# Performance work log

Hardware: AMD Instinct MI355X
Metric: run time of the kernel (lower is better)

Reference implementation:

```python
import jax, jax.numpy as jnp
import numpy as np
from jax import lax

T_LEN, BATCH, D_IN, D_HID, N_LAYERS = 512, 32, 512, 512, 4


def setup_inputs() -> dict:
    key = jax.random.key(0)
    kx, kw, ku = jax.random.split(key, 3)
    x = jax.random.normal(kx, (T_LEN, BATCH, D_IN), dtype=jnp.float32)
    # xavier-ish scale on input kernels to keep the relu recurrence stable
    W = jax.random.normal(kw, (N_LAYERS, D_HID, D_IN), dtype=jnp.float32) * (1.0 / np.sqrt(D_IN))
    b = jnp.zeros((N_LAYERS, D_HID), dtype=jnp.float32)
    # diagonal recurrent weights in [0,1) so |u|<=1 (non-exploding)
    u = jax.random.uniform(ku, (N_LAYERS, D_HID), dtype=jnp.float32)
    return {"x": x, "W": W, "b": b, "u": u}


def _indrnn_layer(x, W_l, b_l, u_l):
    # x: [T, B, Din]; precompute input projection as one big GEMM
    xh = jnp.einsum('tbd,hd->tbh', x, W_l) + b_l  # [T, B, Dh]
    h0 = jnp.zeros((x.shape[1], W_l.shape[0]), dtype=x.dtype)

    def step(h, xh_t):
        h_new = jax.nn.relu(xh_t + u_l * h)
        return h_new, h_new

    _, outs = lax.scan(step, h0, xh)
    return outs  # [T, B, Dh]


def reference(x, W, b, u):
    out = x
    for l in range(W.shape[0]):  # fixed small layer count
        out = _indrnn_layer(out, W[l], b[l], u[l])
    return out
```

## Files before the change

kernel.cpp:

```cpp
#include <hip/hip_runtime.h>
#include <hip/hip_bf16.h>

typedef short bf16x8 __attribute__((ext_vector_type(8)));
typedef float f32x4 __attribute__((ext_vector_type(4)));

#define T_LEN 512
#define BATCH 32
#define D 512
#define M_TOT (T_LEN * BATCH)
#define NLAYER 4

#define BM 128
#define BN 128
#define BK 64
#define NT (D / BK)
#define EP 72

#define CH 32
#define NCH (T_LEN / CH)

__global__ __launch_bounds__(256) void convert_k(const float* __restrict__ W,
                                                 __hip_bfloat16* __restrict__ Wb) {
    const int i = (blockIdx.x * 256 + threadIdx.x) * 4;
    float4 v = *(const float4*)(W + i);
    __hip_bfloat16 h0 = __float2bfloat16(v.x);
    __hip_bfloat16 h1 = __float2bfloat16(v.y);
    __hip_bfloat16 h2 = __float2bfloat16(v.z);
    __hip_bfloat16 h3 = __float2bfloat16(v.w);
    ushort4 o;
    o.x = *(const unsigned short*)&h0;
    o.y = *(const unsigned short*)&h1;
    o.z = *(const unsigned short*)&h2;
    o.w = *(const unsigned short*)&h3;
    *(ushort4*)(Wb + i) = o;
}

template <bool AF32>
__global__ __launch_bounds__(256) void gemm_bt(const void* __restrict__ Avp,
                                               const __hip_bfloat16* __restrict__ Bt,
                                               const float* __restrict__ bias,
                                               __hip_bfloat16* __restrict__ Cb) {
    constexpr int K = D;
    constexpr int N = D;
    __shared__ __hip_bfloat16 smem[4 * BM * BK];
    __hip_bfloat16* const AsP[2] = {smem, smem + BM * BK};
    __hip_bfloat16* const BsP[2] = {smem + 2 * BM * BK, smem + 3 * BM * BK};

    const int tid  = threadIdx.x;
    const int wave = tid >> 6;
    const int lane = tid & 63;

    const int bid = blockIdx.x;
    const int xcd = bid & 7;
    const int jb  = bid >> 3;
    const int bm  = xcd * 16 + (jb >> 2);
    const int bn  = jb & 3;

    const int wm = (wave >> 1) * 64;
    const int wn = (wave & 1) * 64;

    const int srow = lane >> 3;
    const int scol = ((lane & 7) ^ srow) * 8;

    const __hip_bfloat16* Ag = AF32 ? nullptr
                                    : (const __hip_bfloat16*)Avp + (size_t)(bm * BM) * K;
    const float* Agf = AF32 ? (const float*)Avp + (size_t)(bm * BM) * K : nullptr;
    const __hip_bfloat16* Bg = Bt + (size_t)(bn * BN) * K;

    f32x4 acc[4][4] = {};
    float4 va[4][2];

#define STAGE_A_LDS(buf, k0)                                                                         \
    do {                                                                                             \
        _Pragma("unroll") for (int jj = 0; jj < 4; ++jj) {                                           \
            const int rbase = (jj * 4 + wave) * 8;                                                   \
            __builtin_amdgcn_global_load_lds(                                                        \
                (const __attribute__((address_space(1))) void*)(Ag + (size_t)(rbase + srow) * K + (k0) + scol), \
                (__attribute__((address_space(3))) void*)(&AsP[buf][rbase * BK]), 16, 0, 0);         \
        }                                                                                            \
    } while (0)

#define STAGE_B(buf, k0)                                                                             \
    do {                                                                                             \
        _Pragma("unroll") for (int jj = 0; jj < 4; ++jj) {                                           \
            const int rbase = (jj * 4 + wave) * 8;                                                   \
            __builtin_amdgcn_global_load_lds(                                                        \
                (const __attribute__((address_space(1))) void*)(Bg + (size_t)(rbase + srow) * K + (k0) + scol), \
                (__attribute__((address_space(3))) void*)(&BsP[buf][rbase * BK]), 16, 0, 0);         \
        }                                                                                            \
    } while (0)

#define LOAD_A_F32(k0)                                                                               \
    do {                                                                                             \
        _Pragma("unroll") for (int jj = 0; jj < 4; ++jj) {                                           \
            const int rbase = (jj * 4 + wave) * 8;                                                   \
            const float* s = Agf + (size_t)(rbase + srow) * K + (k0) + scol;                         \
            va[jj][0] = *(const float4*)s;                                                           \
            va[jj][1] = *(const float4*)(s + 4);                                                     \
        }                                                                                            \
    } while (0)

#define WRITE_A_F32(buf)                                                                             \
    do {                                                                                             \
        _Pragma("unroll") for (int jj = 0; jj < 4; ++jj) {                                           \
            const int rbase = (jj * 4 + wave) * 8;                                                   \
            bf16x8 pk;                                                                               \
            _Pragma("unroll") for (int q = 0; q < 4; ++q) {                                          \
                __hip_bfloat16 t0 = __float2bfloat16(((const float*)&va[jj][0])[q]);                 \
                __hip_bfloat16 t1 = __float2bfloat16(((const float*)&va[jj][1])[q]);                 \
                pk[q]     = *(const short*)&t0;                                                      \
                pk[q + 4] = *(const short*)&t1;                                                      \
            }                                                                                        \
            *(bf16x8*)(&AsP[buf][(rbase + srow) * BK + (lane & 7) * 8]) = pk;                        \
        }                                                                                            \
    } while (0)

#define COMPUTE(buf)                                                                                 \
    do {                                                                                             \
        bf16x8 af[4][2], bv[4][2];                                                                   \
        const int fr = lane & 15;                                                                    \
        const int kq = lane >> 4;                                                                    \
        _Pragma("unroll") for (int mi = 0; mi < 4; ++mi) {                                           \
            const int r = wm + mi * 16 + fr;                                                         \
            _Pragma("unroll") for (int kh = 0; kh < 2; ++kh) {                                       \
                const int c = ((kh * 4 + kq) ^ (fr & 7)) * 8;                                        \
                af[mi][kh] = *(const bf16x8*)(&AsP[buf][r * BK + c]);                                \
            }                                                                                        \
        }                                                                                            \
        _Pragma("unroll") for (int ni = 0; ni < 4; ++ni) {                                           \
            const int r = wn + ni * 16 + fr;                                                         \
            _Pragma("unroll") for (int kh = 0; kh < 2; ++kh) {                                       \
                const int c = ((kh * 4 + kq) ^ (fr & 7)) * 8;                                        \
                bv[ni][kh] = *(const bf16x8*)(&BsP[buf][r * BK + c]);                                \
            }                                                                                        \
        }                                                                                            \
        _Pragma("unroll") for (int kh = 0; kh < 2; ++kh)                                             \
            _Pragma("unroll") for (int mi = 0; mi < 4; ++mi)                                         \
                _Pragma("unroll") for (int ni = 0; ni < 4; ++ni)                                     \
                    acc[mi][ni] = __builtin_amdgcn_mfma_f32_16x16x32_bf16(af[mi][kh], bv[ni][kh],    \
                                                                          acc[mi][ni], 0, 0, 0);    \
    } while (0)

    if constexpr (AF32) {
        LOAD_A_F32(0);
        STAGE_B(0, 0);
        WRITE_A_F32(0);
        __syncthreads();
        int cur = 0;
#pragma unroll
        for (int kt = 1; kt < NT; ++kt) {
            LOAD_A_F32(kt * BK);
            STAGE_B(cur ^ 1, kt * BK);
            COMPUTE(cur);
            WRITE_A_F32(cur ^ 1);
            __syncthreads();
            cur ^= 1;
        }
        COMPUTE(cur);
    } else {
        STAGE_A_LDS(0, 0);
        STAGE_B(0, 0);
        __syncthreads();
        int cur = 0;
#pragma unroll
        for (int kt = 1; kt < NT; ++kt) {
            STAGE_A_LDS(cur ^ 1, kt * BK);
            STAGE_B(cur ^ 1, kt * BK);
            COMPUTE(cur);
            __syncthreads();
            cur ^= 1;
        }
        COMPUTE(cur);
    }
    __syncthreads();

    {
        __hip_bfloat16* S = smem + wave * (64 * EP);
        const int cfr = lane & 15;
        const int cfq = lane >> 4;
        float bs[4];
#pragma unroll
        for (int ni = 0; ni < 4; ++ni) bs[ni] = bias[bn * BN + wn + ni * 16 + cfr];
#pragma unroll
        for (int mi = 0; mi < 4; ++mi)
#pragma unroll
            for (int ni = 0; ni < 4; ++ni)
#pragma unroll
                for (int r = 0; r < 4; ++r)
                    S[(mi * 16 + cfq * 4 + r) * EP + ni * 16 + cfr] =
                        __float2bfloat16(acc[mi][ni][r] + bs[ni]);
        const int rq = lane >> 3;
        const int cl = (lane & 7) * 8;
#pragma unroll
        for (int p = 0; p < 8; ++p) {
            const int lr = p * 8 + rq;
            bf16x8 v = *(const bf16x8*)(S + lr * EP + cl);
            *(bf16x8*)(&Cb[(size_t)(bm * BM + wm + lr) * N + bn * BN + wn + cl]) = v;
        }
    }
#undef STAGE_A_LDS
#undef STAGE_B
#undef LOAD_A_F32
#undef WRITE_A_F32
#undef COMPUTE
}

template <int MODE>
__global__ __launch_bounds__(512) void scan_k(const __hip_bfloat16* __restrict__ xh,
                                              const float* __restrict__ u,
                                              float* __restrict__ outf,
                                              __hip_bfloat16* __restrict__ outb) {
    __shared__ float4 md[NCH][32];
    const int i2  = threadIdx.x & 31;
    const int c   = threadIdx.x >> 5;
    const int idx = blockIdx.x * 64 + i2 * 2;
    const float u0 = u[idx & (D - 1)];
    const float u1 = u[(idx + 1) & (D - 1)];

    const __hip_bfloat16* p = xh + (size_t)c * CH * M_TOT + idx;
    unsigned int xv[CH];
#pragma unroll
    for (int t = 0; t < CH; ++t) xv[t] = *(const unsigned int*)(p + (size_t)t * M_TOT);

    float m0 = 0.f, d0 = 0.f, m1 = 0.f, d1 = 0.f;
#pragma unroll
    for (int t = 0; t < CH; ++t) {
        const float a0 = __uint_as_float(xv[t] << 16);
        const float a1 = __uint_as_float(xv[t] & 0xffff0000u);
        m0 = fmaxf(fmaf(u0, m0, a0), 0.f);
        d0 = fmaf(u0, d0, a0);
        m1 = fmaxf(fmaf(u1, m1, a1), 0.f);
        d1 = fmaf(u1, d1, a1);
    }
    md[c][i2] = make_float4(m0, d0, m1, d1);
    __syncthreads();

    float e0 = u0 * u0, e1 = u1 * u1;
    e0 *= e0; e0 *= e0; e0 *= e0; e0 *= e0;
    e1 *= e1; e1 *= e1; e1 *= e1; e1 *= e1;
    float h0 = 0.f, h1 = 0.f;
    for (int jj = 0; jj < c; ++jj) {
        const float4 v = md[jj][i2];
        h0 = fmaxf(v.x, fmaf(e0, h0, v.y));
        h1 = fmaxf(v.z, fmaf(e1, h1, v.w));
    }

    const size_t base = (size_t)c * CH * M_TOT + idx;
#pragma unroll
    for (int t = 0; t < CH; ++t) {
        const size_t off = base + (size_t)t * M_TOT;
        const float a0 = __uint_as_float(xv[t] << 16);
        const float a1 = __uint_as_float(xv[t] & 0xffff0000u);
        h0 = fmaxf(fmaf(u0, h0, a0), 0.f);
        h1 = fmaxf(fmaf(u1, h1, a1), 0.f);
        if (MODE & 1) *(float2*)(outf + off) = make_float2(h0, h1);
        if (MODE & 2) {
            __hip_bfloat16 b0 = __float2bfloat16(h0);
            __hip_bfloat16 b1 = __float2bfloat16(h1);
            unsigned int pk = (unsigned int)(*(unsigned short*)&b0) |
                              ((unsigned int)(*(unsigned short*)&b1) << 16);
            *(unsigned int*)(outb + off) = pk;
        }
    }
}

extern "C" void kernel_launch(void* const* d_in, const int* in_sizes, int n_in,
                              void* d_out, int out_size, void* d_ws, size_t ws_size,
                              hipStream_t stream) {
    const float* x = (const float*)d_in[0];
    const float* W = (const float*)d_in[1];
    const float* b = (const float*)d_in[2];
    const float* u = (const float*)d_in[3];
    float* out = (float*)d_out;

    __hip_bfloat16* Wb = (__hip_bfloat16*)d_ws;
    __hip_bfloat16* Ab = (__hip_bfloat16*)((char*)d_ws + (size_t)NLAYER * D * D * 2);
    __hip_bfloat16* Xh = Ab + (size_t)M_TOT * D;

    convert_k<<<(NLAYER * D * D / 4) / 256, 256, 0, stream>>>(W, Wb);

    for (int l = 0; l < NLAYER; ++l) {
        if (l == 0) {
            gemm_bt<true><<<(M_TOT / BM) * (D / BN), 256, 0, stream>>>(
                (const void*)x, Wb, b, Xh);
        } else {
            gemm_bt<false><<<(M_TOT / BM) * (D / BN), 256, 0, stream>>>(
                (const void*)Ab, Wb + (size_t)l * D * D, b + (size_t)l * D, Xh);
        }
        if (l < NLAYER - 1) {
            scan_k<2><<<M_TOT / 64, 512, 0, stream>>>(Xh, u + (size_t)l * D, nullptr, Ab);
        } else {
            scan_k<1><<<M_TOT / 64, 512, 0, stream>>>(Xh, u + (size_t)l * D, out, nullptr);
        }
    }
}
```

Before: 116.3 us.

## Use triple-buffered 128x64 GEMM with explicit vmcnt waits for bf16 layers

Splits the GEMM into a dedicated fp32-input kernel for layer 0 and a new kernel for bf16 layers 1-3. The new kernel uses 128x64 tiles, doubling the block count to 1024. It keeps three LDS stages in flight, loading two tiles ahead and waiting with explicit s_waitcnt vmcnt plus raw barriers instead of a full __syncthreads. The goal is to hide global-to-LDS latency better and improve occupancy and load balance across CUs. The cost is more redundant A-tile loads, since each A tile is now read by 8 column blocks instead of 4.

```diff
diff --git a/kernel.cpp b/kernel.cpp
--- a/kernel.cpp
+++ b/kernel.cpp
@@ -16,8 +16,25 @@
 #define NT (D / BK)
 #define EP 72
 
+#define RBM 128
+#define RBN 64
+#define RSLOT (RBM * BK + RBN * BK)
+#define RSMEM_BYTES (3 * RSLOT * 2)
+#define REP 40
+
 #define CH 32
 #define NCH (T_LEN / CH)
+
+#define SBAR()                             \
+    do {                                   \
+        __builtin_amdgcn_s_barrier();      \
+        __builtin_amdgcn_sched_barrier(0); \
+    } while (0)
+#define VMCNT(n)                                                   \
+    do {                                                           \
+        asm volatile("s_waitcnt vmcnt(" #n ")" ::: "memory");      \
+        __builtin_amdgcn_sched_barrier(0);                         \
+    } while (0)
 
 __global__ __launch_bounds__(256) void convert_k(const float* __restrict__ W,
                                                  __hip_bfloat16* __restrict__ Wb) {
@@ -35,8 +52,7 @@
     *(ushort4*)(Wb + i) = o;
 }
 
-template <bool AF32>
-__global__ __launch_bounds__(256) void gemm_bt(const void* __restrict__ Avp,
+__global__ __launch_bounds__(256) void gemm_l0(const float* __restrict__ Agf0,
                                                const __hip_bfloat16* __restrict__ Bt,
                                                const float* __restrict__ bias,
                                                __hip_bfloat16* __restrict__ Cb) {
@@ -62,25 +78,13 @@
     const int srow = lane >> 3;
     const int scol = ((lane & 7) ^ srow) * 8;
 
-    const __hip_bfloat16* Ag = AF32 ? nullptr
-                                    : (const __hip_bfloat16*)Avp + (size_t)(bm * BM) * K;
-    const float* Agf = AF32 ? (const float*)Avp + (size_t)(bm * BM) * K : nullptr;
+    const float* Agf = Agf0 + (size_t)(bm * BM) * K;
     const __hip_bfloat16* Bg = Bt + (size_t)(bn * BN) * K;
 
     f32x4 acc[4][4] = {};
     float4 va[4][2];
 
-#define STAGE_A_LDS(buf, k0)                                                                         \
-    do {                                                                                             \
-        _Pragma("unroll") for (int jj = 0; jj < 4; ++jj) {                                           \
-            const int rbase = (jj * 4 + wave) * 8;                                                   \
-            __builtin_amdgcn_global_load_lds(                                                        \
-                (const __attribute__((address_space(1))) void*)(Ag + (size_t)(rbase + srow) * K + (k0) + scol), \
-                (__attribute__((address_space(3))) void*)(&AsP[buf][rbase * BK]), 16, 0, 0);         \
-        }                                                                                            \
-    } while (0)
-
-#define STAGE_B(buf, k0)                                                                             \
+#define STAGE_B0(buf, k0)                                                                            \
     do {                                                                                             \
         _Pragma("unroll") for (int jj = 0; jj < 4; ++jj) {                                           \
             const int rbase = (jj * 4 + wave) * 8;                                                   \
@@ -90,7 +94,7 @@
         }                                                                                            \
     } while (0)
 
-#define LOAD_A_F32(k0)                                                                               \
+#define LOAD_A0(k0)                                                                                  \
     do {                                                                                             \
         _Pragma("unroll") for (int jj = 0; jj < 4; ++jj) {                                           \
             const int rbase = (jj * 4 + wave) * 8;                                                   \
@@ -100,7 +104,7 @@
         }                                                                                            \
     } while (0)
 
-#define WRITE_A_F32(buf)                                                                             \
+#define WRITE_A0(buf)                                                                                \
     do {                                                                                             \
         _Pragma("unroll") for (int jj = 0; jj < 4; ++jj) {                                           \
             const int rbase = (jj * 4 + wave) * 8;                                                   \
@@ -115,7 +119,7 @@
         }                                                                                            \
     } while (0)
 
-#define COMPUTE(buf)                                                                                 \
+#define COMPUTE0(buf)                                                                                \
     do {                                                                                             \
         bf16x8 af[4][2], bv[4][2];                                                                   \
         const int fr = lane & 15;                                                                    \
@@ -141,37 +145,21 @@
                                                                           acc[mi][ni], 0, 0, 0);    \
     } while (0)
 
-    if constexpr (AF32) {
-        LOAD_A_F32(0);
-        STAGE_B(0, 0);
-        WRITE_A_F32(0);
+    LOAD_A0(0);
+    STAGE_B0(0, 0);
+    WRITE_A0(0);
+    __syncthreads();
+    int cur = 0;
+#pragma unroll
+    for (int kt = 1; kt < NT; ++kt) {
+        LOAD_A0(kt * BK);
+        STAGE_B0(cur ^ 1, kt * BK);
+        COMPUTE0(cur);
+        WRITE_A0(cur ^ 1);
         __syncthreads();
-        int cur = 0;
-#pragma unroll
-        for (int kt = 1; kt < NT; ++kt) {
-            LOAD_A_F32(kt * BK);
-            STAGE_B(cur ^ 1, kt * BK);
-            COMPUTE(cur);
-            WRITE_A_F32(cur ^ 1);
-            __syncthreads();
-            cur ^= 1;
-        }
-        COMPUTE(cur);
-    } else {
-        STAGE_A_LDS(0, 0);
-        STAGE_B(0, 0);
-        __syncthreads();
-        int cur = 0;
-#pragma unroll
-        for (int kt = 1; kt < NT; ++kt) {
-            STAGE_A_LDS(cur ^ 1, kt * BK);
-            STAGE_B(cur ^ 1, kt * BK);
-            COMPUTE(cur);
-            __syncthreads();
-            cur ^= 1;
-        }
-        COMPUTE(cur);
-    }
+        cur ^= 1;
+    }
+    COMPUTE0(cur);
     __syncthreads();
 
     {
@@ -198,10 +186,132 @@
             *(bf16x8*)(&Cb[(size_t)(bm * BM + wm + lr) * N + bn * BN + wn + cl]) = v;
         }
     }
-#undef STAGE_A_LDS
-#undef STAGE_B
-#undef LOAD_A_F32
-#undef WRITE_A_F32
+#undef STAGE_B0
+#undef LOAD_A0
+#undef WRITE_A0
+#undef COMPUTE0
+}
+
+__global__ __launch_bounds__(256) void gemm_r3(const __hip_bfloat16* __restrict__ A,
+                                               const __hip_bfloat16* __restrict__ Bt,
+                                               const float* __restrict__ bias,
+                                               __hip_bfloat16* __restrict__ Cb) {
+    constexpr int K = D;
+    constexpr int N = D;
+    extern __shared__ __hip_bfloat16 smem[];
+
+    const int tid  = threadIdx.x;
+    const int wave = tid >> 6;
+    const int lane = tid & 63;
+
+    const int bid = blockIdx.x;
+    const int xcd = bid & 7;
+    const int jb  = bid >> 3;
+    const int bm  = xcd * 16 + (jb >> 3);
+    const int bn  = jb & 7;
+
+    const int wm = (wave >> 1) * 64;
+    const int wn = (wave & 1) * 32;
+
+    const int srow = lane >> 3;
+    const int scol = ((lane & 7) ^ srow) * 8;
+
+    const __hip_bfloat16* Ag = A  + (size_t)(bm * RBM) * K;
+    const __hip_bfloat16* Bg = Bt + (size_t)(bn * RBN) * K;
+
+    f32x4 acc[4][2] = {};
+
+#define STAGE(slot, k0)                                                                              \
+    do {                                                                                             \
+        __hip_bfloat16* const Asl = smem + (slot) * RSLOT;                                           \
+        __hip_bfloat16* const Bsl = Asl + RBM * BK;                                                  \
+        _Pragma("unroll") for (int jj = 0; jj < 4; ++jj) {                                           \
+            const int rbase = (wave * 4 + jj) * 8;                                                   \
+            __builtin_amdgcn_global_load_lds(                                                        \
+                (const __attribute__((address_space(1))) void*)(Ag + (size_t)(rbase + srow) * K + (k0) + scol), \
+                (__attribute__((address_space(3))) void*)(Asl + rbase * BK), 16, 0, 0);              \
+        }                                                                                            \
+        _Pragma("unroll") for (int jj = 0; jj < 2; ++jj) {                                           \
+            const int rbase = (wave * 2 + jj) * 8;                                                   \
+            __builtin_amdgcn_global_load_lds(                                                        \
+                (const __attribute__((address_space(1))) void*)(Bg + (size_t)(rbase + srow) * K + (k0) + scol), \
+                (__attribute__((address_space(3))) void*)(Bsl + rbase * BK), 16, 0, 0);              \
+        }                                                                                            \
+    } while (0)
+
+#define COMPUTE(slot)                                                                                \
+    do {                                                                                             \
+        const __hip_bfloat16* const Asl = smem + (slot) * RSLOT;                                     \
+        const __hip_bfloat16* const Bsl = Asl + RBM * BK;                                            \
+        bf16x8 af[4][2], bv[2][2];                                                                   \
+        const int fr = lane & 15;                                                                    \
+        const int kq = lane >> 4;                                                                    \
+        _Pragma("unroll") for (int mi = 0; mi < 4; ++mi) {                                           \
+            const int r = wm + mi * 16 + fr;                                                         \
+            _Pragma("unroll") for (int kh = 0; kh < 2; ++kh) {                                       \
+                const int c = ((kh * 4 + kq) ^ (fr & 7)) * 8;                                        \
+                af[mi][kh] = *(const bf16x8*)(&Asl[r * BK + c]);                                     \
+            }                                                                                        \
+        }                                                                                            \
+        _Pragma("unroll") for (int ni = 0; ni < 2; ++ni) {                                           \
+            const int r = wn + ni * 16 + fr;                                                         \
+            _Pragma("unroll") for (int kh = 0; kh < 2; ++kh) {                                       \
+                const int c = ((kh * 4 + kq) ^ (fr & 7)) * 8;                                        \
+                bv[ni][kh] = *(const bf16x8*)(&Bsl[r * BK + c]);                                     \
+            }                                                                                        \
+        }                                                                                            \
+        _Pragma("unroll") for (int kh = 0; kh < 2; ++kh)                                             \
+            _Pragma("unroll") for (int mi = 0; mi < 4; ++mi)                                         \
+                _Pragma("unroll") for (int ni = 0; ni < 2; ++ni)                                     \
+                    acc[mi][ni] = __builtin_amdgcn_mfma_f32_16x16x32_bf16(af[mi][kh], bv[ni][kh],    \
+                                                                          acc[mi][ni], 0, 0, 0);    \
+    } while (0)
+
+    STAGE(0, 0);
+    STAGE(1, BK);
+    VMCNT(6);
+    SBAR();
+
+#pragma unroll
+    for (int t = 0; t < NT; ++t) {
+        if (t + 2 < NT) STAGE((t + 2) % 3, (t + 2) * BK);
+        COMPUTE(t % 3);
+        if (t < NT - 1) {
+            if (t + 2 < NT) {
+                VMCNT(6);
+            } else {
+                VMCNT(0);
+            }
+            SBAR();
+        }
+    }
+    __syncthreads();
+
+    {
+        __hip_bfloat16* S = smem + wave * (64 * REP);
+        const int cfr = lane & 15;
+        const int cfq = lane >> 4;
+        float bs[2];
+#pragma unroll
+        for (int ni = 0; ni < 2; ++ni) bs[ni] = bias[bn * RBN + wn + ni * 16 + cfr];
+#pragma unroll
+        for (int mi = 0; mi < 4; ++mi)
+#pragma unroll
+            for (int ni = 0; ni < 2; ++ni)
+#pragma unroll
+                for (int r = 0; r < 4; ++r)
+                    S[(mi * 16 + cfq * 4 + r) * REP + ni * 16 + cfr] =
+                        __float2bfloat16(acc[mi][ni][r] + bs[ni]);
+        const int rq = lane >> 2;
+        const int cl = (lane & 3) * 8;
+#pragma unroll
+        for (int p = 0; p < 4; ++p) {
+            const int lr = p * 16 + rq;
+            bf16x8 v = *(const bf16x8*)(S + lr * REP + cl);
+            *(bf16x8*)(&Cb[(size_t)(bm * RBM + wm + lr) * N + bn * RBN + wn + cl]) = v;
+        }
+    }
+#undef STAGE
 #undef COMPUTE
 }
 
@@ -277,15 +387,17 @@
     __hip_bfloat16* Ab = (__hip_bfloat16*)((char*)d_ws + (size_t)NLAYER * D * D * 2);
     __hip_bfloat16* Xh = Ab + (size_t)M_TOT * D;
 
+    (void)hipFuncSetAttribute((const void*)gemm_r3,
+                              hipFuncAttributeMaxDynamicSharedMemorySize, RSMEM_BYTES);
+
     convert_k<<<(NLAYER * D * D / 4) / 256, 256, 0, stream>>>(W, Wb);
 
     for (int l = 0; l < NLAYER; ++l) {
         if (l == 0) {
-            gemm_bt<true><<<(M_TOT / BM) * (D / BN), 256, 0, stream>>>(
-                (const void*)x, Wb, b, Xh);
+            gemm_l0<<<(M_TOT / BM) * (D / BN), 256, 0, stream>>>(x, Wb, b, Xh);
         } else {
-            gemm_bt<false><<<(M_TOT / BM) * (D / BN), 256, 0, stream>>>(
-                (const void*)Ab, Wb + (size_t)l * D * D, b + (size_t)l * D, Xh);
+            gemm_r3<<<(M_TOT / RBM) * (D / RBN), 256, RSMEM_BYTES, stream>>>(
+                Ab, Wb + (size_t)l * D * D, b + (size_t)l * D, Xh);
         }
         if (l < NLAYER - 1) {
             scan_k<2><<<M_TOT / 64, 512, 0, stream>>>(Xh, u + (size_t)l * D, nullptr, Ab);
```

Result: no change. 116.2 us (-0.1%).
